# Kernel tuning notes

Hardware: AMD Instinct MI355X
Metric: run time of the kernel (lower is better)

## Reference

```python
import jax, jax.numpy as jnp
import numpy as np

D_MODEL = 1024
NUM_HEADS = 16
HEAD_DIM = D_MODEL // NUM_HEADS


def setup_inputs() -> dict:
    key = jax.random.key(0)
    ks = jax.random.split(key, 10)
    B, S, D = 2, 2048, D_MODEL
    s = 1.0 / np.sqrt(D)
    return {
        "x": jax.random.normal(ks[0], (B, S, D), dtype=jnp.float32),
        "q_w": jax.random.normal(ks[1], (D, D), dtype=jnp.float32) * s,
        "q_b": jnp.zeros((D,), dtype=jnp.float32),
        "k_w": jax.random.normal(ks[2], (D, D), dtype=jnp.float32) * s,
        "k_b": jnp.zeros((D,), dtype=jnp.float32),
        "v_w": jax.random.normal(ks[3], (D, D), dtype=jnp.float32) * s,
        "v_b": jnp.zeros((D,), dtype=jnp.float32),
        "out_w": jax.random.normal(ks[4], (D, D), dtype=jnp.float32) * s,
        "out_b": jnp.zeros((D,), dtype=jnp.float32),
        "evidence_scale": jnp.ones((1,), dtype=jnp.float32),
        "evidence_bias": jnp.zeros((1,), dtype=jnp.float32),
    }


def reference(x, q_w, q_b, k_w, k_b, v_w, v_b, out_w, out_b, evidence_scale, evidence_bias):
    B, S, D = x.shape
    H, Hd = NUM_HEADS, HEAD_DIM

    def proj(w, b):  # torch Linear: x @ w.T + b, then split heads -> [B,H,S,Hd]
        y = jnp.einsum('bsd,ed->bse', x, w) + b
        return y.reshape(B, S, H, Hd).transpose(0, 2, 1, 3)

    Q = proj(q_w, q_b)
    K = proj(k_w, k_b)
    V = proj(v_w, v_b)

    scores = jnp.einsum('bhqd,bhkd->bhqk', Q, K) / np.sqrt(Hd)  # [B,H,S,S]
    evidence = jnp.exp(scores) * evidence_scale + 1.0 + evidence_bias
    denom = evidence.sum(axis=-1, keepdims=True)                # [B,H,S,1]
    uncertainty = S / denom                                     # [B,H,S,1]
    probs = evidence / denom

    attn = jnp.einsum('bhqk,bhkd->bhqd', probs, V)              # [B,H,S,Hd]
    attn = attn.transpose(0, 2, 1, 3).reshape(B, S, D)
    output = jnp.einsum('bsd,ed->bse', attn, out_w) + out_b
    return output, jnp.squeeze(uncertainty, -1)
```

## Files before the change

### kernel.cpp

```cpp
#include <hip/hip_runtime.h>

typedef __attribute__((ext_vector_type(8))) short bf16x8;
typedef __attribute__((ext_vector_type(4))) float f32x4;

constexpr int Dm  = 1024;
constexpr int NH  = 16;
constexpr int HD  = 64;
constexpr int SQ  = 2048;
constexpr int BB  = 2;
constexpr int MM  = BB * SQ;

__device__ __forceinline__ unsigned short f2bf(float f) {
    unsigned int u = __float_as_uint(f);
    u += 0x7FFFu + ((u >> 16) & 1u);
    return (unsigned short)(u >> 16);
}

__device__ __forceinline__ void gld16(const void* g, void* l) {
    __builtin_amdgcn_global_load_lds(
        (const __attribute__((address_space(1))) void*)g,
        (__attribute__((address_space(3))) void*)l, 16, 0, 0);
}

__global__ void cast_all(const float4* __restrict__ x,  const float4* __restrict__ qw,
                         const float4* __restrict__ kw, const float4* __restrict__ vw,
                         const float4* __restrict__ ow,
                         uint2* __restrict__ xb,  uint2* __restrict__ qwb,
                         uint2* __restrict__ kwb, uint2* __restrict__ vwb,
                         uint2* __restrict__ owb)
{
    int i = blockIdx.x * 256 + threadIdx.x;
    const float4* src; uint2* dst; int off;
    if      (i < 1048576) { src = x;  dst = xb;  off = i; }
    else if (i < 1310720) { src = qw; dst = qwb; off = i - 1048576; }
    else if (i < 1572864) { src = kw; dst = kwb; off = i - 1310720; }
    else if (i < 1835008) { src = vw; dst = vwb; off = i - 1572864; }
    else                  { src = ow; dst = owb; off = i - 1835008; }
    float4 v = src[off];
    uint2 o;
    o.x = (unsigned)f2bf(v.x) | ((unsigned)f2bf(v.y) << 16);
    o.y = (unsigned)f2bf(v.z) | ((unsigned)f2bf(v.w) << 16);
    dst[off] = o;
}

template<typename EPI>
__device__ __forceinline__ void gemm_core(const unsigned short* __restrict__ A,
                                          const unsigned short* __restrict__ W,
                                          const float* __restrict__ bias,
                                          int n0, int m0, EPI epi)
{
    __shared__ unsigned short As[128 * 32];
    __shared__ unsigned short Ws[128 * 32];
    const int t    = threadIdx.x;
    const int lane = t & 63, w = t >> 6;
    const int lm   = lane & 15, quad = lane >> 4;
    const int wm   = w & 1, wn = w >> 1;

    const f32x4 fz = {0.f, 0.f, 0.f, 0.f};
    f32x4 acc[4][4];
#pragma unroll
    for (int mi = 0; mi < 4; ++mi)
#pragma unroll
        for (int ni = 0; ni < 4; ++ni) acc[mi][ni] = fz;

    float bsv[4];
#pragma unroll
    for (int ni = 0; ni < 4; ++ni) bsv[ni] = bias[n0 + wn * 64 + ni * 16 + lm];

    const int r0 = t >> 2,         ks0 = t & 3;
    const int r1 = (t + 256) >> 2, ks1 = (t + 256) & 3;

    for (int k0 = 0; k0 < 1024; k0 += 32) {
        __syncthreads();
        gld16(A + (size_t)(m0 + r0) * 1024 + k0 + ks0 * 8, &As[t * 8]);
        gld16(A + (size_t)(m0 + r1) * 1024 + k0 + ks1 * 8, &As[(t + 256) * 8]);
        gld16(W + (size_t)(n0 + r0) * 1024 + k0 + ks0 * 8, &Ws[t * 8]);
        gld16(W + (size_t)(n0 + r1) * 1024 + k0 + ks1 * 8, &Ws[(t + 256) * 8]);
        __syncthreads();

        bf16x8 af[4], bfr[4];
#pragma unroll
        for (int mi = 0; mi < 4; ++mi)
            af[mi] = *(const bf16x8*)&As[(wm * 64 + mi * 16 + lm) * 32 + quad * 8];
#pragma unroll
        for (int ni = 0; ni < 4; ++ni)
            bfr[ni] = *(const bf16x8*)&Ws[(wn * 64 + ni * 16 + lm) * 32 + quad * 8];
#pragma unroll
        for (int mi = 0; mi < 4; ++mi)
#pragma unroll
            for (int ni = 0; ni < 4; ++ni)
                acc[mi][ni] = __builtin_amdgcn_mfma_f32_16x16x32_bf16(
                                  af[mi], bfr[ni], acc[mi][ni], 0, 0, 0);
    }

#pragma unroll
    for (int mi = 0; mi < 4; ++mi)
#pragma unroll
        for (int ni = 0; ni < 4; ++ni)
#pragma unroll
            for (int r = 0; r < 4; ++r) {
                const int m = m0 + wm * 64 + mi * 16 + quad * 4 + r;
                const int n = n0 + wn * 64 + ni * 16 + lm;
                epi(m, n, acc[mi][ni][r] + bsv[ni]);
            }
}

__global__ __launch_bounds__(256) void gemm_qkv(
    const unsigned short* __restrict__ xb,
    const unsigned short* __restrict__ qwb, const float* __restrict__ qb,
    const unsigned short* __restrict__ kwb, const float* __restrict__ kb,
    const unsigned short* __restrict__ vwb, const float* __restrict__ vb,
    unsigned short* __restrict__ Qb, unsigned short* __restrict__ Kb,
    unsigned short* __restrict__ Vb)
{
    const int z = blockIdx.z;
    const unsigned short* W = (z == 0) ? qwb : (z == 1) ? kwb : vwb;
    const float* bias       = (z == 0) ? qb  : (z == 1) ? kb  : vb;
    unsigned short* dst     = (z == 0) ? Qb  : (z == 1) ? Kb  : Vb;
    const int n0 = blockIdx.x * 128, m0 = blockIdx.y * 128;
    const bool vt = (z == 2);

    gemm_core(xb, W, bias, n0, m0, [&](int m, int n, float v) {
        const int b = m >> 11, s = m & 2047, h = n >> 6, hd = n & 63;
        const size_t idx = vt ? ((size_t)((b * NH + h) * 64 + hd) * SQ + s)
                              : ((size_t)((b * NH + h) * SQ + s) * 64 + hd);
        dst[idx] = f2bf(v);
    });
}

__global__ __launch_bounds__(256) void gemm_out(
    const unsigned short* __restrict__ Ab, const unsigned short* __restrict__ owb,
    const float* __restrict__ ob, float* __restrict__ out)
{
    const int n0 = blockIdx.x * 128, m0 = blockIdx.y * 128;
    gemm_core(Ab, owb, ob, n0, m0, [&](int m, int n, float v) {
        out[(size_t)m * 1024 + n] = v;
    });
}

constexpr int ST = 88;

__global__ __launch_bounds__(256) void attn_mfma(const unsigned short* __restrict__ Qg,
                                                 const unsigned short* __restrict__ Kg,
                                                 const unsigned short* __restrict__ Vtg,
                                                 const float* __restrict__ esc,
                                                 const float* __restrict__ ebi,
                                                 unsigned short* __restrict__ Ab,
                                                 float* __restrict__ unc)
{
    __shared__ unsigned short Qs[64 * ST];
    __shared__ unsigned short Ks[64 * ST];
    __shared__ unsigned short Vts[64 * ST];
    __shared__ unsigned short Es[4 * 16 * ST];
    __shared__ float dred[64][17];
    __shared__ float dinv[64];

    const int t    = threadIdx.x;
    const int lane = t & 63, w = t >> 6;
    const int lm   = lane & 15, quad = lane >> 4;
    const int qt   = blockIdx.x & 31;
    const int bh   = blockIdx.x >> 5;
    const int q0   = qt * 64;

    const float scale = esc[0];
    const float bias1 = 1.0f + ebi[0];

    {
        const unsigned short* g = Qg + (size_t)(bh * SQ + q0) * 64;
#pragma unroll
        for (int i = 0; i < 2; ++i) {
            int seg = t + 256 * i, r = seg >> 3, c8 = seg & 7;
            *(uint4*)&Qs[r * ST + c8 * 8] = *(const uint4*)(g + r * 64 + c8 * 8);
        }
    }

    const f32x4 fz = {0.f, 0.f, 0.f, 0.f};
    f32x4 acc[4];
#pragma unroll
    for (int ni = 0; ni < 4; ++ni) acc[ni] = fz;
    float drow[4] = {0.f, 0.f, 0.f, 0.f};

    for (int kt = 0; kt < 32; ++kt) {
        __syncthreads();
        {
            const unsigned short* kg = Kg  + (size_t)(bh * SQ + kt * 64) * 64;
            const unsigned short* vg = Vtg + (size_t)bh * 64 * SQ + kt * 64;
#pragma unroll
            for (int i = 0; i < 2; ++i) {
                int seg = t + 256 * i, r = seg >> 3, c8 = seg & 7;
                *(uint4*)&Ks[r * ST + c8 * 8]  = *(const uint4*)(kg + r * 64 + c8 * 8);
                *(uint4*)&Vts[r * ST + c8 * 8] = *(const uint4*)(vg + (size_t)r * SQ + c8 * 8);
            }
        }
        __syncthreads();

        bf16x8 qa[2];
#pragma unroll
        for (int kc = 0; kc < 2; ++kc)
            qa[kc] = *(const bf16x8*)&Qs[(w * 16 + lm) * ST + kc * 32 + quad * 8];
#pragma unroll
        for (int ni = 0; ni < 4; ++ni) {
            f32x4 s = fz;
#pragma unroll
            for (int kc = 0; kc < 2; ++kc) {
                bf16x8 kb = *(const bf16x8*)&Ks[(ni * 16 + lm) * ST + kc * 32 + quad * 8];
                s = __builtin_amdgcn_mfma_f32_16x16x32_bf16(qa[kc], kb, s, 0, 0, 0);
            }
#pragma unroll
            for (int r = 0; r < 4; ++r) {
                float ev = __expf(s[r] * 0.125f) * scale + bias1;
                drow[r] += ev;
                Es[w * 16 * ST + (quad * 4 + r) * ST + ni * 16 + lm] = f2bf(ev);
            }
        }
        __syncthreads();

        bf16x8 ea[2];
#pragma unroll
        for (int kc = 0; kc < 2; ++kc)
            ea[kc] = *(const bf16x8*)&Es[w * 16 * ST + lm * ST + kc * 32 + quad * 8];
#pragma unroll
        for (int ni = 0; ni < 4; ++ni)
#pragma unroll
            for (int kc = 0; kc < 2; ++kc) {
                bf16x8 vb = *(const bf16x8*)&Vts[(ni * 16 + lm) * ST + kc * 32 + quad * 8];
                acc[ni] = __builtin_amdgcn_mfma_f32_16x16x32_bf16(ea[kc], vb, acc[ni], 0, 0, 0);
            }
    }

    __syncthreads();
#pragma unroll
    for (int r = 0; r < 4; ++r)
        dred[w * 16 + quad * 4 + r][lm] = drow[r];
    __syncthreads();
    if (t < 64) {
        float d = 0.f;
#pragma unroll
        for (int c = 0; c < 16; ++c) d += dred[t][c];
        unc[(size_t)bh * SQ + q0 + t] = (float)SQ / d;
        dinv[t] = 1.0f / d;
    }
    __syncthreads();

    const int b = bh >> 4, h = bh & 15;
#pragma unroll
    for (int ni = 0; ni < 4; ++ni)
#pragma unroll
        for (int r = 0; r < 4; ++r) {
            const int q = w * 16 + quad * 4 + r;
            const float v = acc[ni][r] * dinv[q];
            Ab[(size_t)(b * SQ + q0 + q) * Dm + h * 64 + ni * 16 + lm] = f2bf(v);
        }
}

extern "C" void kernel_launch(void* const* d_in, const int* in_sizes, int n_in,
                              void* d_out, int out_size, void* d_ws, size_t ws_size,
                              hipStream_t stream)
{
    const float* x   = (const float*)d_in[0];
    const float* qw  = (const float*)d_in[1];
    const float* qb  = (const float*)d_in[2];
    const float* kw  = (const float*)d_in[3];
    const float* kb  = (const float*)d_in[4];
    const float* vw  = (const float*)d_in[5];
    const float* vb  = (const float*)d_in[6];
    const float* ow  = (const float*)d_in[7];
    const float* ob  = (const float*)d_in[8];
    const float* esc = (const float*)d_in[9];
    const float* ebi = (const float*)d_in[10];

    float* out = (float*)d_out;
    float* unc = out + (size_t)MM * Dm;

    unsigned short* xb  = (unsigned short*)d_ws;
    unsigned short* qwb = (unsigned short*)((char*)d_ws + (8u  << 20));
    unsigned short* kwb = (unsigned short*)((char*)d_ws + (10u << 20));
    unsigned short* vwb = (unsigned short*)((char*)d_ws + (12u << 20));
    unsigned short* owb = (unsigned short*)((char*)d_ws + (14u << 20));
    unsigned short* Vb  = (unsigned short*)((char*)d_ws + (16u << 20));
    unsigned short* Ab  = xb;

    unsigned short* Qb = (unsigned short*)d_out;
    unsigned short* Kb = Qb + (size_t)MM * Dm;

    cast_all<<<dim3(2097152 / 256), dim3(256), 0, stream>>>(
        (const float4*)x, (const float4*)qw, (const float4*)kw,
        (const float4*)vw, (const float4*)ow,
        (uint2*)xb, (uint2*)qwb, (uint2*)kwb, (uint2*)vwb, (uint2*)owb);

    gemm_qkv<<<dim3(Dm / 128, MM / 128, 3), dim3(256), 0, stream>>>(
        xb, qwb, qb, kwb, kb, vwb, vb, Qb, Kb, Vb);

    attn_mfma<<<dim3(BB * NH * (SQ / 64)), dim3(256), 0, stream>>>(
        Qb, Kb, Vb, esc, ebi, Ab, unc);

    gemm_out<<<dim3(Dm / 128, MM / 128), dim3(256), 0, stream>>>(Ab, owb, ob, out);
}
```

Measured before the change: 249.8 us.

## Double-buffer GEMM and attention tiles, shrink out-proj tile, shuffle-reduce denominators

New measurement: 224.5 us. 10.1% less time.

```diff
diff --git a/kernel.cpp b/kernel.cpp
--- a/kernel.cpp
+++ b/kernel.cpp
@@ -2,6 +2,7 @@
 
 typedef __attribute__((ext_vector_type(8))) short bf16x8;
 typedef __attribute__((ext_vector_type(4))) float f32x4;
+typedef unsigned short ushort_t;
 
 constexpr int Dm  = 1024;
 constexpr int NH  = 16;
@@ -10,10 +11,10 @@
 constexpr int BB  = 2;
 constexpr int MM  = BB * SQ;
 
-__device__ __forceinline__ unsigned short f2bf(float f) {
+__device__ __forceinline__ ushort_t f2bf(float f) {
     unsigned int u = __float_as_uint(f);
     u += 0x7FFFu + ((u >> 16) & 1u);
-    return (unsigned short)(u >> 16);
+    return (ushort_t)(u >> 16);
 }
 
 __device__ __forceinline__ void gld16(const void* g, void* l) {
@@ -43,23 +44,24 @@
     dst[off] = o;
 }
 
-template<typename EPI>
-__device__ __forceinline__ void gemm_core(const unsigned short* __restrict__ A,
-                                          const unsigned short* __restrict__ W,
+template<int TM, typename EPI>
+__device__ __forceinline__ void gemm_core(const ushort_t* __restrict__ A,
+                                          const ushort_t* __restrict__ W,
                                           const float* __restrict__ bias,
                                           int n0, int m0, EPI epi)
 {
-    __shared__ unsigned short As[128 * 32];
-    __shared__ unsigned short Ws[128 * 32];
+    constexpr int AF = TM / 32;
+    __shared__ ushort_t As[2][TM * 32];
+    __shared__ ushort_t Ws[2][128 * 32];
     const int t    = threadIdx.x;
     const int lane = t & 63, w = t >> 6;
     const int lm   = lane & 15, quad = lane >> 4;
     const int wm   = w & 1, wn = w >> 1;
 
     const f32x4 fz = {0.f, 0.f, 0.f, 0.f};
-    f32x4 acc[4][4];
-#pragma unroll
-    for (int mi = 0; mi < 4; ++mi)
+    f32x4 acc[AF][4];
+#pragma unroll
+    for (int mi = 0; mi < AF; ++mi)
 #pragma unroll
         for (int ni = 0; ni < 4; ++ni) acc[mi][ni] = fz;
 
@@ -67,60 +69,68 @@
 #pragma unroll
     for (int ni = 0; ni < 4; ++ni) bsv[ni] = bias[n0 + wn * 64 + ni * 16 + lm];
 
-    const int r0 = t >> 2,         ks0 = t & 3;
-    const int r1 = (t + 256) >> 2, ks1 = (t + 256) & 3;
-
+    auto stage = [&](int k0, int b) {
+#pragma unroll
+        for (int j = 0; j < TM / 64; ++j) {
+            int s = t + 256 * j;
+            gld16(A + (size_t)(m0 + (s >> 2)) * 1024 + k0 + (s & 3) * 8, &As[b][s * 8]);
+        }
+#pragma unroll
+        for (int j = 0; j < 2; ++j) {
+            int s = t + 256 * j;
+            gld16(W + (size_t)(n0 + (s >> 2)) * 1024 + k0 + (s & 3) * 8, &Ws[b][s * 8]);
+        }
+    };
+
+    stage(0, 0);
+    int cur = 0;
     for (int k0 = 0; k0 < 1024; k0 += 32) {
         __syncthreads();
-        gld16(A + (size_t)(m0 + r0) * 1024 + k0 + ks0 * 8, &As[t * 8]);
-        gld16(A + (size_t)(m0 + r1) * 1024 + k0 + ks1 * 8, &As[(t + 256) * 8]);
-        gld16(W + (size_t)(n0 + r0) * 1024 + k0 + ks0 * 8, &Ws[t * 8]);
-        gld16(W + (size_t)(n0 + r1) * 1024 + k0 + ks1 * 8, &Ws[(t + 256) * 8]);
-        __syncthreads();
-
-        bf16x8 af[4], bfr[4];
-#pragma unroll
-        for (int mi = 0; mi < 4; ++mi)
-            af[mi] = *(const bf16x8*)&As[(wm * 64 + mi * 16 + lm) * 32 + quad * 8];
+        if (k0 + 32 < 1024) stage(k0 + 32, cur ^ 1);
+
+        bf16x8 af[AF], bfr[4];
+#pragma unroll
+        for (int mi = 0; mi < AF; ++mi)
+            af[mi] = *(const bf16x8*)&As[cur][(wm * (TM / 2) + mi * 16 + lm) * 32 + quad * 8];
 #pragma unroll
         for (int ni = 0; ni < 4; ++ni)
-            bfr[ni] = *(const bf16x8*)&Ws[(wn * 64 + ni * 16 + lm) * 32 + quad * 8];
-#pragma unroll
-        for (int mi = 0; mi < 4; ++mi)
+            bfr[ni] = *(const bf16x8*)&Ws[cur][(wn * 64 + ni * 16 + lm) * 32 + quad * 8];
+#pragma unroll
+        for (int mi = 0; mi < AF; ++mi)
 #pragma unroll
             for (int ni = 0; ni < 4; ++ni)
                 acc[mi][ni] = __builtin_amdgcn_mfma_f32_16x16x32_bf16(
                                   af[mi], bfr[ni], acc[mi][ni], 0, 0, 0);
+        cur ^= 1;
     }
 
 #pragma unroll
-    for (int mi = 0; mi < 4; ++mi)
+    for (int mi = 0; mi < AF; ++mi)
 #pragma unroll
         for (int ni = 0; ni < 4; ++ni)
 #pragma unroll
             for (int r = 0; r < 4; ++r) {
-                const int m = m0 + wm * 64 + mi * 16 + quad * 4 + r;
+                const int m = m0 + wm * (TM / 2) + mi * 16 + quad * 4 + r;
                 const int n = n0 + wn * 64 + ni * 16 + lm;
                 epi(m, n, acc[mi][ni][r] + bsv[ni]);
             }
 }
 
 __global__ __launch_bounds__(256) void gemm_qkv(
-    const unsigned short* __restrict__ xb,
-    const unsigned short* __restrict__ qwb, const float* __restrict__ qb,
-    const unsigned short* __restrict__ kwb, const float* __restrict__ kb,
-    const unsigned short* __restrict__ vwb, const float* __restrict__ vb,
-    unsigned short* __restrict__ Qb, unsigned short* __restrict__ Kb,
-    unsigned short* __restrict__ Vb)
+    const ushort_t* __restrict__ xb,
+    const ushort_t* __restrict__ qwb, const float* __restrict__ qb,
+    const ushort_t* __restrict__ kwb, const float* __restrict__ kb,
+    const ushort_t* __restrict__ vwb, const float* __restrict__ vb,
+    ushort_t* __restrict__ Qb, ushort_t* __restrict__ Kb, ushort_t* __restrict__ Vb)
 {
     const int z = blockIdx.z;
-    const unsigned short* W = (z == 0) ? qwb : (z == 1) ? kwb : vwb;
-    const float* bias       = (z == 0) ? qb  : (z == 1) ? kb  : vb;
-    unsigned short* dst     = (z == 0) ? Qb  : (z == 1) ? Kb  : Vb;
+    const ushort_t* W   = (z == 0) ? qwb : (z == 1) ? kwb : vwb;
+    const float*    bias = (z == 0) ? qb  : (z == 1) ? kb  : vb;
+    ushort_t*       dst  = (z == 0) ? Qb  : (z == 1) ? Kb  : Vb;
     const int n0 = blockIdx.x * 128, m0 = blockIdx.y * 128;
     const bool vt = (z == 2);
 
-    gemm_core(xb, W, bias, n0, m0, [&](int m, int n, float v) {
+    gemm_core<128>(xb, W, bias, n0, m0, [&](int m, int n, float v) {
         const int b = m >> 11, s = m & 2047, h = n >> 6, hd = n & 63;
         const size_t idx = vt ? ((size_t)((b * NH + h) * 64 + hd) * SQ + s)
                               : ((size_t)((b * NH + h) * SQ + s) * 64 + hd);
@@ -129,31 +139,26 @@
 }
 
 __global__ __launch_bounds__(256) void gemm_out(
-    const unsigned short* __restrict__ Ab, const unsigned short* __restrict__ owb,
+    const ushort_t* __restrict__ Ab, const ushort_t* __restrict__ owb,
     const float* __restrict__ ob, float* __restrict__ out)
 {
-    const int n0 = blockIdx.x * 128, m0 = blockIdx.y * 128;
-    gemm_core(Ab, owb, ob, n0, m0, [&](int m, int n, float v) {
+    const int n0 = blockIdx.x * 128, m0 = blockIdx.y * 64;
+    gemm_core<64>(Ab, owb, ob, n0, m0, [&](int m, int n, float v) {
         out[(size_t)m * 1024 + n] = v;
     });
 }
 
-constexpr int ST = 88;
-
-__global__ __launch_bounds__(256) void attn_mfma(const unsigned short* __restrict__ Qg,
-                                                 const unsigned short* __restrict__ Kg,
-                                                 const unsigned short* __restrict__ Vtg,
+__global__ __launch_bounds__(256) void attn_mfma(const ushort_t* __restrict__ Qg,
+                                                 const ushort_t* __restrict__ Kg,
+                                                 const ushort_t* __restrict__ Vtg,
                                                  const float* __restrict__ esc,
                                                  const float* __restrict__ ebi,
-                                                 unsigned short* __restrict__ Ab,
+                                                 ushort_t* __restrict__ Ab,
                                                  float* __restrict__ unc)
 {
-    __shared__ unsigned short Qs[64 * ST];
-    __shared__ unsigned short Ks[64 * ST];
-    __shared__ unsigned short Vts[64 * ST];
-    __shared__ unsigned short Es[4 * 16 * ST];
-    __shared__ float dred[64][17];
-    __shared__ float dinv[64];
+    __shared__ __align__(16) ushort_t Kbuf[2][4096];
+    __shared__ __align__(16) ushort_t Vbuf[2][4096];
+    __shared__ __align__(16) ushort_t Es[4][16 * 40];
 
     const int t    = threadIdx.x;
     const int lane = t & 63, w = t >> 6;
@@ -165,91 +170,90 @@
     const float scale = esc[0];
     const float bias1 = 1.0f + ebi[0];
 
-    {
-        const unsigned short* g = Qg + (size_t)(bh * SQ + q0) * 64;
-#pragma unroll
-        for (int i = 0; i < 2; ++i) {
-            int seg = t + 256 * i, r = seg >> 3, c8 = seg & 7;
-            *(uint4*)&Qs[r * ST + c8 * 8] = *(const uint4*)(g + r * 64 + c8 * 8);
-        }
-    }
+    bf16x8 qa[2];
+#pragma unroll
+    for (int kc = 0; kc < 2; ++kc)
+        qa[kc] = *(const bf16x8*)(Qg + (size_t)(bh * SQ + q0 + w * 16 + lm) * 64
+                                  + kc * 32 + quad * 8);
 
     const f32x4 fz = {0.f, 0.f, 0.f, 0.f};
     f32x4 acc[4];
 #pragma unroll
-    for (int ni = 0; ni < 4; ++ni) acc[ni] = fz;
+    for (int nd = 0; nd < 4; ++nd) acc[nd] = fz;
     float drow[4] = {0.f, 0.f, 0.f, 0.f};
 
+    auto stage = [&](int kt, int b) {
+        const ushort_t* kg = Kg + (size_t)(bh * SQ + kt * 64 + w * 16 + lm) * 64 + quad * 8;
+        gld16(kg,      &Kbuf[b][(w * 2 + 0) * 512]);
+        gld16(kg + 32, &Kbuf[b][(w * 2 + 1) * 512]);
+        const ushort_t* vg = Vtg + (size_t)bh * 64 * SQ + (size_t)(w * 16 + lm) * SQ
+                           + kt * 64 + quad * 8;
+        gld16(vg,      &Vbuf[b][(w * 2 + 0) * 512]);
+        gld16(vg + 32, &Vbuf[b][(w * 2 + 1) * 512]);
+    };
+
+    stage(0, 0);
+    int cur = 0;
     for (int kt = 0; kt < 32; ++kt) {
         __syncthreads();
-        {
-            const unsigned short* kg = Kg  + (size_t)(bh * SQ + kt * 64) * 64;
-            const unsigned short* vg = Vtg + (size_t)bh * 64 * SQ + kt * 64;
-#pragma unroll
-            for (int i = 0; i < 2; ++i) {
-                int seg = t + 256 * i, r = seg >> 3, c8 = seg & 7;
-                *(uint4*)&Ks[r * ST + c8 * 8]  = *(const uint4*)(kg + r * 64 + c8 * 8);
-                *(uint4*)&Vts[r * ST + c8 * 8] = *(const uint4*)(vg + (size_t)r * SQ + c8 * 8);
+        if (kt + 1 < 32) stage(kt + 1, cur ^ 1);
+        const ushort_t* Kc = Kbuf[cur];
+        const ushort_t* Vc = Vbuf[cur];
+        ushort_t* EsW = &Es[w][0];
+
+#pragma unroll
+        for (int hc = 0; hc < 2; ++hc) {
+#pragma unroll
+            for (int ni = 0; ni < 2; ++ni) {
+                f32x4 s = fz;
+#pragma unroll
+                for (int kc = 0; kc < 2; ++kc) {
+                    bf16x8 kb = *(const bf16x8*)&Kc[((hc * 2 + ni) * 2 + kc) * 512 + lane * 8];
+                    s = __builtin_amdgcn_mfma_f32_16x16x32_bf16(qa[kc], kb, s, 0, 0, 0);
+                }
+#pragma unroll
+                for (int r = 0; r < 4; ++r) {
+                    float ev = __expf(s[r] * 0.125f) * scale + bias1;
+                    drow[r] += ev;
+                    EsW[(quad * 4 + r) * 40 + ni * 16 + lm] = f2bf(ev);
+                }
+            }
+            bf16x8 ea = *(const bf16x8*)&EsW[lm * 40 + quad * 8];
+#pragma unroll
+            for (int nd = 0; nd < 4; ++nd) {
+                bf16x8 vb = *(const bf16x8*)&Vc[(nd * 2 + hc) * 512 + lane * 8];
+                acc[nd] = __builtin_amdgcn_mfma_f32_16x16x32_bf16(ea, vb, acc[nd], 0, 0, 0);
             }
         }
-        __syncthreads();
-
-        bf16x8 qa[2];
-#pragma unroll
-        for (int kc = 0; kc < 2; ++kc)
-            qa[kc] = *(const bf16x8*)&Qs[(w * 16 + lm) * ST + kc * 32 + quad * 8];
-#pragma unroll
-        for (int ni = 0; ni < 4; ++ni) {
-            f32x4 s = fz;
-#pragma unroll
-            for (int kc = 0; kc < 2; ++kc) {
-                bf16x8 kb = *(const bf16x8*)&Ks[(ni * 16 + lm) * ST + kc * 32 + quad * 8];
-                s = __builtin_amdgcn_mfma_f32_16x16x32_bf16(qa[kc], kb, s, 0, 0, 0);
-            }
-#pragma unroll
-            for (int r = 0; r < 4; ++r) {
-                float ev = __expf(s[r] * 0.125f) * scale + bias1;
-                drow[r] += ev;
-                Es[w * 16 * ST + (quad * 4 + r) * ST + ni * 16 + lm] = f2bf(ev);
-            }
-        }
-        __syncthreads();
-
-        bf16x8 ea[2];
-#pragma unroll
-        for (int kc = 0; kc < 2; ++kc)
-            ea[kc] = *(const bf16x8*)&Es[w * 16 * ST + lm * ST + kc * 32 + quad * 8];
-#pragma unroll
-        for (int ni = 0; ni < 4; ++ni)
-#pragma unroll
-            for (int kc = 0; kc < 2; ++kc) {
-                bf16x8 vb = *(const bf16x8*)&Vts[(ni * 16 + lm) * ST + kc * 32 + quad * 8];
-                acc[ni] = __builtin_amdgcn_mfma_f32_16x16x32_bf16(ea[kc], vb, acc[ni], 0, 0, 0);
-            }
+        cur ^= 1;
     }
 
-    __syncthreads();
-#pragma unroll
-    for (int r = 0; r < 4; ++r)
-        dred[w * 16 + quad * 4 + r][lm] = drow[r];
-    __syncthreads();
-    if (t < 64) {
-        float d = 0.f;
-#pragma unroll
-        for (int c = 0; c < 16; ++c) d += dred[t][c];
-        unc[(size_t)bh * SQ + q0 + t] = (float)SQ / d;
-        dinv[t] = 1.0f / d;
+#pragma unroll
+    for (int r = 0; r < 4; ++r) {
+        float d = drow[r];
+        d += __shfl_xor(d, 1, 64);
+        d += __shfl_xor(d, 2, 64);
+        d += __shfl_xor(d, 4, 64);
+        d += __shfl_xor(d, 8, 64);
+        drow[r] = d;
     }
-    __syncthreads();
+    if (lm == 0) {
+#pragma unroll
+        for (int r = 0; r < 4; ++r)
+            unc[(size_t)bh * SQ + q0 + w * 16 + quad * 4 + r] = (float)SQ / drow[r];
+    }
 
     const int b = bh >> 4, h = bh & 15;
-#pragma unroll
-    for (int ni = 0; ni < 4; ++ni)
+    float di[4];
+#pragma unroll
+    for (int r = 0; r < 4; ++r) di[r] = 1.0f / drow[r];
+#pragma unroll
+    for (int nd = 0; nd < 4; ++nd)
 #pragma unroll
         for (int r = 0; r < 4; ++r) {
             const int q = w * 16 + quad * 4 + r;
-            const float v = acc[ni][r] * dinv[q];
-            Ab[(size_t)(b * SQ + q0 + q) * Dm + h * 64 + ni * 16 + lm] = f2bf(v);
+            Ab[(size_t)(b * SQ + q0 + q) * Dm + h * 64 + nd * 16 + lm]
+                = f2bf(acc[nd][r] * di[r]);
         }
 }
 
@@ -272,16 +276,16 @@
     float* out = (float*)d_out;
     float* unc = out + (size_t)MM * Dm;
 
-    unsigned short* xb  = (unsigned short*)d_ws;
-    unsigned short* qwb = (unsigned short*)((char*)d_ws + (8u  << 20));
-    unsigned short* kwb = (unsigned short*)((char*)d_ws + (10u << 20));
-    unsigned short* vwb = (unsigned short*)((char*)d_ws + (12u << 20));
-    unsigned short* owb = (unsigned short*)((char*)d_ws + (14u << 20));
-    unsigned short* Vb  = (unsigned short*)((char*)d_ws + (16u << 20));
-    unsigned short* Ab  = xb;
-
-    unsigned short* Qb = (unsigned short*)d_out;
-    unsigned short* Kb = Qb + (size_t)MM * Dm;
+    ushort_t* xb  = (ushort_t*)d_ws;
+    ushort_t* qwb = (ushort_t*)((char*)d_ws + (8u  << 20));
+    ushort_t* kwb = (ushort_t*)((char*)d_ws + (10u << 20));
+    ushort_t* vwb = (ushort_t*)((char*)d_ws + (12u << 20));
+    ushort_t* owb = (ushort_t*)((char*)d_ws + (14u << 20));
+    ushort_t* Vb  = (ushort_t*)((char*)d_ws + (16u << 20));
+    ushort_t* Ab  = xb;
+
+    ushort_t* Qb = (ushort_t*)d_out;
+    ushort_t* Kb = Qb + (size_t)MM * Dm;
 
     cast_all<<<dim3(2097152 / 256), dim3(256), 0, stream>>>(
         (const float4*)x, (const float4*)qw, (const float4*)kw,
@@ -294,5 +298,5 @@
     attn_mfma<<<dim3(BB * NH * (SQ / 64)), dim3(256), 0, stream>>>(
         Qb, Kb, Vb, esc, ebi, Ab, unc);
 
-    gemm_out<<<dim3(Dm / 128, MM / 128), dim3(256), 0, stream>>>(Ab, owb, ob, out);
-}
+    gemm_out<<<dim3(Dm / 128, MM / 64), dim3(256), 0, stream>>>(Ab, owb, ob, out);
+}
```
